# Performance work log

Hardware: AMD Instinct MI355X
Metric: run time of the kernel (lower is better)

## Reference

```python
import jax, jax.numpy as jnp
import numpy as np
from jax import lax

B, S, D, G, V = 32, 8, 128, 32, 64   # batch, slots, hidden_dim, grid_size, vocab_size
K, ED = 128, 32                       # VQ codebook size, code dim


def _conv(x, w, b, pad):
    # standard Conv2d, NCHW / OIHW
    y = lax.conv_general_dilated(x, w, (1, 1), [(pad, pad), (pad, pad)],
                                 dimension_numbers=('NCHW', 'OIHW', 'NCHW'))
    return y + b[None, :, None, None]


def _convT(x, w, b):
    # ConvTranspose2d(k=5, stride=1, padding=2) == conv with spatially flipped
    # kernel, padding k-1-p = 2, channels swapped (IOHW layout of torch weight).
    y = lax.conv_general_dilated(x, jnp.flip(w, (2, 3)), (1, 1), [(2, 2), (2, 2)],
                                 dimension_numbers=('NCHW', 'IOHW', 'NCHW'))
    return y + b[None, :, None, None]


def _build_grid(h, w):
    ys = jnp.linspace(0.0, 1.0, h)
    xs = jnp.linspace(0.0, 1.0, w)
    gy, gx = jnp.meshgrid(ys, xs, indexing='ij')
    g = jnp.stack([gy, gx], axis=-1)                 # [H,W,2]
    return jnp.concatenate([g, 1.0 - g], axis=-1)    # [H,W,4]


def setup_inputs() -> dict:
    key = jax.random.key(0)
    ks = jax.random.split(key, 20)
    sc = 0.05
    n = lambda k, sh: jax.random.normal(k, sh, jnp.float32) * sc
    return {
        'latent': jax.random.normal(ks[0], (B, S, D), jnp.float32),
        'pos_w': n(ks[1], (D, 4)),            # Linear(4, hidden): [out,in]
        'pos_b': jnp.zeros((D,), jnp.float32),
        'ct1_w': n(ks[2], (D, 64, 5, 5)),     # ConvTranspose2d: [in,out,kH,kW]
        'ct1_b': jnp.zeros((64,), jnp.float32),
        'ct2_w': n(ks[3], (64, 32, 5, 5)),
        'ct2_b': jnp.zeros((32,), jnp.float32),
        'codebook': jax.random.uniform(ks[4], (K, ED), jnp.float32, -1.0 / K, 1.0 / K),
        'c1_w': n(ks[5], (64, 32, 3, 3)),     # Conv2d: [out,in,kH,kW]
        'c1_b': jnp.zeros((64,), jnp.float32),
        'c2_w': n(ks[6], (V, 64, 3, 3)),
        'c2_b': jnp.zeros((V,), jnp.float32),
        'a1_w': n(ks[7], (64, 32, 3, 3)),
        'a1_b': jnp.zeros((64,), jnp.float32),
        'a2_w': n(ks[8], (1, 64, 3, 3)),
        'a2_b': jnp.zeros((1,), jnp.float32),
    }


def _forward(latent, pos_w, pos_b, ct1_w, ct1_b, ct2_w, ct2_b, codebook,
             c1_w, c1_b, c2_w, c2_b, a1_w, a1_b, a2_w, a2_b):
    b, s, d = latent.shape
    # spatial broadcast of slot latents -> [B*S, D, H, W]
    z = jnp.broadcast_to(latent.reshape(b * s, d, 1, 1), (b * s, d, G, G))
    # soft position embedding
    grid = _build_grid(G, G)                                  # [H,W,4]
    pos = (grid @ pos_w.T + pos_b).transpose(2, 0, 1)[None]   # [1,D,H,W]
    z = z + pos
    # ConvTranspose decoder
    h = jax.nn.relu(_convT(z, ct1_w, ct1_b))
    feat = jax.nn.relu(_convT(h, ct2_w, ct2_b))               # [B*S,32,H,W]
    # VQ bottleneck on channel-last features
    fp = feat.transpose(0, 2, 3, 1)                           # [B*S,H,W,32]
    flat = fp.reshape(-1, ED)                                 # [N,32]
    dist = (jnp.sum(flat * flat, axis=1, keepdims=True)
            + jnp.sum(codebook * codebook, axis=1)
            - 2.0 * flat @ codebook.T)                        # [N,K]
    idx = jnp.argmin(dist, axis=1)                            # [N]
    q = codebook[idx].reshape(fp.shape)                       # gather lookup
    e_loss = jnp.mean((lax.stop_gradient(q) - fp) ** 2)
    q_loss = jnp.mean((q - lax.stop_gradient(fp)) ** 2)
    vq_loss = q_loss + 0.25 * e_loss
    q_ste = fp + lax.stop_gradient(q - fp)                    # straight-through
    vq_feat = q_ste.transpose(0, 3, 1, 2)                     # [B*S,32,H,W]
    # heads
    colors = _conv(jax.nn.silu(_conv(vq_feat, c1_w, c1_b, 1)), c2_w, c2_b, 1)
    colors = colors.reshape(b, s, V, G, G)
    alphas = _conv(jax.nn.silu(_conv(feat, a1_w, a1_b, 1)), a2_w, a2_b, 1)
    alphas = alphas.reshape(b, s, 1, G, G)
    alphas_n = jax.nn.softmax(alphas, axis=1)
    recon = jnp.sum(alphas_n * colors, axis=1)                # [B,V,H,W]
    return recon, alphas_n, vq_loss


def reference(latent, pos_w, pos_b, ct1_w, ct1_b, ct2_w, ct2_b, codebook,
              c1_w, c1_b, c2_w, c2_b, a1_w, a1_b, a2_w, a2_b):
    return _forward(latent, pos_w, pos_b, ct1_w, ct1_b, ct2_w, ct2_b, codebook,
                    c1_w, c1_b, c2_w, c2_b, a1_w, a1_b, a2_w, a2_b)
```

## Files before the change

### kernel.cpp

```cpp
#include <hip/hip_runtime.h>
#include <math.h>

#define AOFF 2097152
#define LOFF 2359296

typedef __attribute__((ext_vector_type(8))) short short8;
typedef __attribute__((ext_vector_type(4))) float f32x4;

__device__ __forceinline__ int clsf(int v) { return v < 2 ? v : (v > 29 ? v - 27 : 2); }

__device__ __forceinline__ unsigned int f2bfu(float x) {
    unsigned int u = __float_as_uint(x);
    return (u + 0x7FFFu + ((u >> 16) & 1u)) >> 16;
}
__device__ __forceinline__ unsigned int cvt2(float a, float b) {
    return f2bfu(a) | (f2bfu(b) << 16);
}
__device__ __forceinline__ float bf2f(unsigned short u) {
    return __uint_as_float(((unsigned int)u) << 16);
}

__global__ void w1t_kernel(const float* __restrict__ w1, float* __restrict__ w1t) {
    int idx = blockIdx.x * 256 + threadIdx.x;
    if (idx >= 204800) return;
    int tap = idx % 25, rest = idx / 25;
    w1t[tap * 8192 + rest] = w1[idx];
}

__global__ void tapabc_kernel(const float* __restrict__ pw, const float* __restrict__ pb,
                              const float* __restrict__ w1t, float* __restrict__ tapabc) {
    __shared__ float A3[384];
    int tap = blockIdx.x, t = threadIdx.x;
    if (t < 128) {
        float p0 = pw[t * 4], p1 = pw[t * 4 + 1], p2 = pw[t * 4 + 2], p3 = pw[t * 4 + 3];
        A3[t] = p2 + p3 + pb[t];
        A3[128 + t] = p0 - p2;
        A3[256 + t] = p1 - p3;
    }
    __syncthreads();
    int o = t & 63, comp = t >> 6;
    const float* wp = w1t + tap * 8192 + o;
    const float* a = A3 + comp * 128;
    float s = 0.f;
    for (int i = 0; i < 128; ++i) s = fmaf(wp[i * 64], a[i], s);
    tapabc[(tap * 64 + o) * 3 + comp] = s;
}

__global__ void pfill_kernel(const float* __restrict__ tapabc, const float* __restrict__ b1,
                             float* __restrict__ P2) {
    __shared__ float uv[75];
    int o = blockIdx.x, t = threadIdx.x;
    if (t < 75) {
        int cls = t / 3, comp = t % 3;
        int cy = cls / 5, cx = cls % 5;
        const int klo[5] = {2, 1, 0, 0, 0}, khi[5] = {4, 4, 4, 3, 2};
        const float inv31 = 1.f / 31.f;
        float s = (comp == 0) ? b1[o] : 0.f;
        for (int ky = klo[cy]; ky <= khi[cy]; ++ky)
            for (int kx = klo[cx]; kx <= khi[cx]; ++kx) {
                int tap = (4 - ky) * 5 + (4 - kx);
                const float* tp = &tapabc[(tap * 64 + o) * 3];
                if (comp == 0) s += tp[0] + tp[1] * (ky - 2) * inv31 + tp[2] * (kx - 2) * inv31;
                else if (comp == 1) s += tp[1] * inv31;
                else s += tp[2] * inv31;
            }
        uv[t] = s;
    }
    __syncthreads();
    int y = t >> 5, x = t & 31;
    int cls = clsf(y) * 5 + clsf(x);
    float val = uv[cls * 3] + uv[cls * 3 + 1] * y + uv[cls * 3 + 2] * x;
    P2[((o >> 1) << 11) + (t << 1) + (o & 1)] = val;
}

__global__ void wsum_kernel(const float* __restrict__ w1, float* __restrict__ Wsum) {
    int idx = blockIdx.x * 256 + threadIdx.x;
    if (idx >= 25 * 128 * 64) return;
    int cls = idx >> 13;
    int i = (idx >> 6) & 127;
    int o = idx & 63;
    int cy = cls / 5, cx = cls % 5;
    const int klo[5] = {2, 1, 0, 0, 0}, khi[5] = {4, 4, 4, 3, 2};
    float s = 0.f;
    for (int ky = klo[cy]; ky <= khi[cy]; ++ky)
        for (int kx = klo[cx]; kx <= khi[cx]; ++kx)
            s += w1[(i * 64 + o) * 25 + (4 - ky) * 5 + (4 - kx)];
    Wsum[idx] = s;
}

__global__ void m_kernel(const float* __restrict__ latent, const float* __restrict__ Wsum,
                         float* __restrict__ M) {
    int n = blockIdx.x, cls = blockIdx.y, o = threadIdx.x;
    const float* l = &latent[n * 128];
    const float* w = &Wsum[cls * 8192 + o];
    float a0 = 0.f, a1 = 0.f;
    for (int i = 0; i < 128; i += 2) {
        a0 = fmaf(l[i], w[i * 64], a0);
        a1 = fmaf(l[i + 1], w[(i + 1) * 64], a1);
    }
    M[(n * 25 + cls) * 64 + o] = a0 + a1;
}

__global__ void prep_all_kernel(const float* __restrict__ a1w, const float* __restrict__ c1w,
                                const float* __restrict__ c2w, const float* __restrict__ ct2w,
                                short* __restrict__ wtall) {
    int gid = blockIdx.x * 256 + threadIdx.x;
    if (gid < 36864) {
        const float* src = gid < 18432 ? a1w : c1w;
        int idx = gid < 18432 ? gid : gid - 18432;
        int j = idx & 7, fi = idx >> 3;
        int o = fi % 64, g = (fi / 64) & 3, t = fi / 256;
        int i = g * 8 + j;
        wtall[gid] = (short)f2bfu(src[(o * 32 + i) * 9 + (t / 3) * 3 + (t % 3)]);
    } else if (gid < 73728) {
        int idx = gid - 36864;
        int j = idx & 7, fi = idx >> 3;
        int o = fi % 64, g = (fi / 64) & 3, ks = (fi / 256) & 1, t = fi / 512;
        int i = ks * 32 + g * 8 + j;
        wtall[gid] = (short)f2bfu(c2w[(o * 64 + i) * 9 + (t / 3) * 3 + (t % 3)]);
    } else if (gid < 124928) {
        int idx = gid - 73728;
        int j = idx & 7, fi = idx >> 3;
        int o = fi & 31, g = (fi >> 5) & 3, ks = (fi >> 7) & 1, t = fi >> 8;
        int i = ks * 32 + g * 8 + j;
        int ky = t / 5, kx = t % 5;
        wtall[gid] = (short)f2bfu(ct2w[((i * 32 + o) * 5 + (4 - ky)) * 5 + (4 - kx)]);
    }
}

__global__ __launch_bounds__(256) void conv5_kernel(
        const float* __restrict__ M, const float* __restrict__ P2,
        const short* __restrict__ wt, const float* __restrict__ b2,
        unsigned short* __restrict__ featb) {
    __shared__ __align__(16) short tile[12 * 36 * 40];
    __shared__ float Ml[1600];
    const int n = blockIdx.x, y0 = blockIdx.y * 8;
    const int tid = threadIdx.x, w = tid >> 6, l = tid & 63;
    const int lx = l & 15, lg = l >> 4;

    for (int e = tid; e < 1600; e += 256) Ml[e] = M[n * 1600 + e];
    __syncthreads();

    f32x4 acc[2][2][2];
    #pragma unroll
    for (int m = 0; m < 2; ++m)
        #pragma unroll
        for (int q = 0; q < 2; ++q)
            #pragma unroll
            for (int c = 0; c < 2; ++c) acc[m][q][c] = (f32x4){0.f, 0.f, 0.f, 0.f};

    #pragma unroll 1
    for (int ks = 0; ks < 2; ++ks) {
        if (ks) __syncthreads();
        for (int e = tid; e < 6912; e += 256) {
            int cx = e % 36;
            int q = e / 36;
            int ipl = q & 15;
            int r = q >> 4;
            int gy = y0 - 2 + r, gx = cx - 2;
            unsigned int pack = 0u;
            if (gy >= 0 && gy < 32 && gx >= 0 && gx < 32) {
                int cls = clsf(gy) * 5 + clsf(gx);
                int pp = gy * 32 + gx;
                float2 pv = ((const float2*)P2)[((ks * 16 + ipl) << 10) + pp];
                float2 ml = ((const float2*)Ml)[cls * 32 + ks * 16 + ipl];
                pack = cvt2(fmaxf(ml.x + pv.x, 0.f), fmaxf(ml.y + pv.y, 0.f));
            }
            *(unsigned int*)((char*)tile + (r * 36 + cx) * 80 + ipl * 4) = pack;
        }
        __syncthreads();
        for (int kx = 0; kx < 5; ++kx) {
            short8 af[5][2];
            #pragma unroll
            for (int ky = 0; ky < 5; ++ky)
                #pragma unroll
                for (int m = 0; m < 2; ++m)
                    af[ky][m] = *(const short8*)(wt + (ky * 5 + kx) * 2048 +
                                                 ((ks * 4 + lg) * 32 + m * 16 + lx) * 8);
            #pragma unroll
            for (int colf = 0; colf < 2; ++colf) {
                const int cbase = ((2 * w) * 36 + kx + colf * 16 + lx) * 80 + lg * 16;
                short8 bc[6];
                #pragma unroll
                for (int ir = 0; ir < 6; ++ir)
                    bc[ir] = *(const short8*)((char*)tile + cbase + ir * (36 * 80));
                #pragma unroll
                for (int ky = 0; ky < 5; ++ky)
                    #pragma unroll
                    for (int q = 0; q < 2; ++q)
                        #pragma unroll
                        for (int m = 0; m < 2; ++m)
                            acc[m][q][colf] = __builtin_amdgcn_mfma_f32_16x16x32_bf16(
                                af[ky][m], bc[q + ky], acc[m][q][colf], 0, 0, 0);
            }
        }
    }

    #pragma unroll
    for (int m = 0; m < 2; ++m)
        #pragma unroll
        for (int q = 0; q < 2; ++q)
            #pragma unroll
            for (int colf = 0; colf < 2; ++colf) {
                int yl = 2 * w + q, x = colf * 16 + lx;
                unsigned long long pk = 0ull;
                #pragma unroll
                for (int r = 0; r < 4; ++r) {
                    int och = m * 16 + lg * 4 + r;
                    float v = fmaxf(acc[m][q][colf][r] + b2[och], 0.f);
                    pk |= (unsigned long long)f2bfu(v) << (16 * r);
                }
                *(unsigned long long*)(featb + (n * 1024 + (y0 + yl) * 32 + x) * 32
                                       + m * 16 + lg * 4) = pk;
            }
}

template<int ACT>
__global__ __launch_bounds__(256, 6) void conv3_kernel(
        const unsigned short* __restrict__ in_, const short* __restrict__ wt,
        const float* __restrict__ bias, unsigned short* __restrict__ out_) {
    __shared__ __align__(16) short smem[6 * 34 * 40];
    const int n = blockIdx.x, y0 = blockIdx.y * 4;
    const int tid = threadIdx.x, w = tid >> 6, l = tid & 63;
    const int lx = l & 15, lg = l >> 4;

    for (int e = tid; e < 816; e += 256) {
        int px = e >> 2, qc = e & 3;
        int r = px / 34, cx = px - r * 34;
        int gy = y0 - 1 + r, gx = cx - 1;
        short8 v8 = (short8){0, 0, 0, 0, 0, 0, 0, 0};
        if (gy >= 0 && gy < 32 && gx >= 0 && gx < 32)
            v8 = *(const short8*)(in_ + (n * 1024 + gy * 32 + gx) * 32 + qc * 8);
        *(short8*)((char*)smem + px * 80 + qc * 16) = v8;
    }
    __syncthreads();

    f32x4 acc[4][2];
    #pragma unroll
    for (int m = 0; m < 4; ++m)
        #pragma unroll
        for (int c = 0; c < 2; ++c) acc[m][c] = (f32x4){0.f, 0.f, 0.f, 0.f};

    #pragma unroll
    for (int kx = 0; kx < 3; ++kx) {
        short8 bc[2][3];
        #pragma unroll
        for (int colf = 0; colf < 2; ++colf) {
            const int cbase = (w * 34 + kx + colf * 16 + lx) * 80 + lg * 16;
            #pragma unroll
            for (int ir = 0; ir < 3; ++ir)
                bc[colf][ir] = *(const short8*)((char*)smem + cbase + ir * (34 * 80));
        }
        #pragma unroll
        for (int m = 0; m < 4; ++m) {
            short8 af[3];
            #pragma unroll
            for (int ky = 0; ky < 3; ++ky)
                af[ky] = *(const short8*)(wt + (ky * 3 + kx) * 2048 +
                                          (lg * 64 + m * 16 + lx) * 8);
            #pragma unroll
            for (int ky = 0; ky < 3; ++ky)
                #pragma unroll
                for (int colf = 0; colf < 2; ++colf)
                    acc[m][colf] = __builtin_amdgcn_mfma_f32_16x16x32_bf16(
                        af[ky], bc[colf][ky], acc[m][colf], 0, 0, 0);
        }
    }

    #pragma unroll
    for (int m = 0; m < 4; ++m)
        #pragma unroll
        for (int colf = 0; colf < 2; ++colf) {
            int x = colf * 16 + lx;
            unsigned long long pk = 0ull;
            #pragma unroll
            for (int r = 0; r < 4; ++r) {
                int och = m * 16 + lg * 4 + r;
                float v = acc[m][colf][r] + bias[och];
                if (ACT == 1) v = v / (1.f + expf(-v));
                pk |= (unsigned long long)f2bfu(v) << (16 * r);
            }
            *(unsigned long long*)(out_ + (n * 1024 + (y0 + w) * 32 + x) * 64
                                   + m * 16 + lg * 4) = pk;
        }
}

__global__ __launch_bounds__(256) void c2_kernel(
        const unsigned short* __restrict__ in_, const short* __restrict__ wt,
        const float* __restrict__ bias, unsigned short* __restrict__ out_) {
    __shared__ __align__(16) short smem[10 * 34 * 40];
    const int n = blockIdx.x, y0 = blockIdx.y * 8;
    const int tid = threadIdx.x, w = tid >> 6, l = tid & 63;
    const int lx = l & 15, lg = l >> 4;

    short8 r0[6], r1[6];
    int pxv[6], qcv[6];
    #pragma unroll
    for (int it = 0; it < 6; ++it) {
        int e = tid + it * 256;
        int px = e >> 2, qc = e & 3;
        pxv[it] = px; qcv[it] = qc;
        short8 v0 = (short8){0, 0, 0, 0, 0, 0, 0, 0};
        short8 v1 = v0;
        if (e < 1360) {
            int r = px / 34, cx = px - r * 34;
            int gy = y0 - 1 + r, gx = cx - 1;
            if (gy >= 0 && gy < 32 && gx >= 0 && gx < 32) {
                const unsigned short* p = in_ + (n * 1024 + gy * 32 + gx) * 64 + qc * 8;
                v0 = *(const short8*)p;
                v1 = *(const short8*)(p + 32);
            }
        }
        r0[it] = v0; r1[it] = v1;
    }
    #pragma unroll
    for (int it = 0; it < 6; ++it)
        if (tid + it * 256 < 1360)
            *(short8*)((char*)smem + pxv[it] * 80 + qcv[it] * 16) = r0[it];
    __syncthreads();

    f32x4 acc[4][2][2];
    #pragma unroll
    for (int m = 0; m < 4; ++m)
        #pragma unroll
        for (int q = 0; q < 2; ++q)
            #pragma unroll
            for (int c = 0; c < 2; ++c) acc[m][q][c] = (f32x4){0.f, 0.f, 0.f, 0.f};

    #pragma unroll
    for (int kx = 0; kx < 3; ++kx) {
        short8 af[3][4];
        #pragma unroll
        for (int ky = 0; ky < 3; ++ky)
            #pragma unroll
            for (int m = 0; m < 4; ++m)
                af[ky][m] = *(const short8*)(wt + (ky * 3 + kx) * 4096 +
                                             (lg * 64 + m * 16 + lx) * 8);
        #pragma unroll
        for (int colf = 0; colf < 2; ++colf) {
            const int cbase = ((2 * w) * 34 + kx + colf * 16 + lx) * 80 + lg * 16;
            short8 bc[4];
            #pragma unroll
            for (int ir = 0; ir < 4; ++ir)
                bc[ir] = *(const short8*)((char*)smem + cbase + ir * (34 * 80));
            #pragma unroll
            for (int ky = 0; ky < 3; ++ky)
                #pragma unroll
                for (int q = 0; q < 2; ++q)
                    #pragma unroll
                    for (int m = 0; m < 4; ++m)
                        acc[m][q][colf] = __builtin_amdgcn_mfma_f32_16x16x32_bf16(
                            af[ky][m], bc[q + ky], acc[m][q][colf], 0, 0, 0);
        }
    }
    __syncthreads();
    #pragma unroll
    for (int it = 0; it < 6; ++it)
        if (tid + it * 256 < 1360)
            *(short8*)((char*)smem + pxv[it] * 80 + qcv[it] * 16) = r1[it];
    __syncthreads();
    #pragma unroll
    for (int kx = 0; kx < 3; ++kx) {
        short8 af[3][4];
        #pragma unroll
        for (int ky = 0; ky < 3; ++ky)
            #pragma unroll
            for (int m = 0; m < 4; ++m)
                af[ky][m] = *(const short8*)(wt + (ky * 3 + kx) * 4096 +
                                             ((4 + lg) * 64 + m * 16 + lx) * 8);
        #pragma unroll
        for (int colf = 0; colf < 2; ++colf) {
            const int cbase = ((2 * w) * 34 + kx + colf * 16 + lx) * 80 + lg * 16;
            short8 bc[4];
            #pragma unroll
            for (int ir = 0; ir < 4; ++ir)
                bc[ir] = *(const short8*)((char*)smem + cbase + ir * (34 * 80));
            #pragma unroll
            for (int ky = 0; ky < 3; ++ky)
                #pragma unroll
                for (int q = 0; q < 2; ++q)
                    #pragma unroll
                    for (int m = 0; m < 4; ++m)
                        acc[m][q][colf] = __builtin_amdgcn_mfma_f32_16x16x32_bf16(
                            af[ky][m], bc[q + ky], acc[m][q][colf], 0, 0, 0);
        }
    }

    #pragma unroll
    for (int m = 0; m < 4; ++m)
        #pragma unroll
        for (int q = 0; q < 2; ++q)
            #pragma unroll
            for (int colf = 0; colf < 2; ++colf) {
                int yl = 2 * w + q, x = colf * 16 + lx;
                unsigned long long pk = 0ull;
                #pragma unroll
                for (int r = 0; r < 4; ++r) {
                    int och = m * 16 + lg * 4 + r;
                    float v = acc[m][q][colf][r] + bias[och];
                    pk |= (unsigned long long)f2bfu(v) << (16 * r);
                }
                *(unsigned long long*)(out_ + (n * 1024 + (y0 + yl) * 32 + x) * 64
                                       + m * 16 + lg * 4) = pk;
            }
}

__global__ void a2dot_kernel(const unsigned short* __restrict__ in, const float* __restrict__ w,
                             float* __restrict__ s9) {
    __shared__ float wl[576];
    int t = threadIdx.x;
    for (int e = t; e < 576; e += 256) wl[e] = w[e];
    __syncthreads();
    int p = blockIdx.x * 256 + t;
    float acc[9];
    #pragma unroll
    for (int k = 0; k < 9; ++k) acc[k] = 0.f;
    const unsigned short* ip = in + (long long)p * 64;
    #pragma unroll
    for (int c8 = 0; c8 < 8; ++c8) {
        short8 v8 = *(const short8*)(ip + c8 * 8);
        #pragma unroll
        for (int j = 0; j < 8; ++j) {
            float v = bf2f((unsigned short)v8[j]);
            #pragma unroll
            for (int k = 0; k < 9; ++k) acc[k] = fmaf(v, wl[(c8 * 8 + j) * 9 + k], acc[k]);
        }
    }
    #pragma unroll
    for (int k = 0; k < 9; ++k) s9[(k << 18) + p] = acc[k];
}

__global__ void a2soft_kernel(const float* __restrict__ s9, const float* __restrict__ b2,
                              float* __restrict__ outp) {
    int idx = blockIdx.x * 256 + threadIdx.x;
    if (idx >= 32 * 1024) return;
    int bb = idx >> 10, yx = idx & 1023;
    int y = yx >> 5, x = yx & 31;
    float v[8];
    float bias = b2[0];
    #pragma unroll
    for (int s = 0; s < 8; ++s) {
        int n = bb * 8 + s;
        float a = bias;
        #pragma unroll
        for (int ky = 0; ky < 3; ++ky) {
            int yy = y + ky - 1;
            if (yy < 0 || yy > 31) continue;
            #pragma unroll
            for (int kx = 0; kx < 3; ++kx) {
                int xx = x + kx - 1;
                if (xx < 0 || xx > 31) continue;
                a += s9[((ky * 3 + kx) << 18) + (n << 10) + yy * 32 + xx];
            }
        }
        v[s] = a;
    }
    float m = -3.4e38f;
    #pragma unroll
    for (int s = 0; s < 8; ++s) m = fmaxf(m, v[s]);
    float sum = 0.f;
    #pragma unroll
    for (int s = 0; s < 8; ++s) { v[s] = expf(v[s] - m); sum += v[s]; }
    float inv = 1.f / sum;
    #pragma unroll
    for (int s = 0; s < 8; ++s) outp[AOFF + ((bb * 8 + s) << 10) + yx] = v[s] * inv;
}

__global__ __launch_bounds__(256) void vq_mfma_kernel(
        const unsigned short* __restrict__ featb, const float* __restrict__ codebook,
        unsigned short* __restrict__ qfeat, float* __restrict__ partial) {
    __shared__ float cbf[4096];
    __shared__ __align__(16) short cbh[4096];
    __shared__ float cn[128];
    __shared__ float red[4];
    const int tid = threadIdx.x;
    const int w = tid >> 6, l = tid & 63;
    const int lx = l & 15, lg = l >> 4;

    for (int e = tid; e < 4096; e += 256) {
        float v = codebook[e];
        cbf[e] = v;
        int code = e >> 5, d = e & 31;
        int off = (code * 32 + d) * 2;
        off ^= (code & 7) << 4;
        *(short*)((char*)cbh + off) = (short)f2bfu(v);
    }
    __syncthreads();
    if (tid < 128) {
        float s = 0.f;
        #pragma unroll
        for (int c = 0; c < 32; ++c) { float v = cbf[tid * 32 + c]; s = fmaf(v, v, s); }
        cn[tid] = s;
    }
    short8 af[8];
    #pragma unroll
    for (int m = 0; m < 8; ++m) {
        int code = m * 16 + lx;
        int off = (code * 32 + lg * 8) * 2;
        off ^= (code & 7) << 4;
        af[m] = *(const short8*)((char*)cbh + off);
    }
    __syncthreads();
    float cnh[8][4];
    #pragma unroll
    for (int m = 0; m < 8; ++m)
        #pragma unroll
        for (int r = 0; r < 4; ++r)
            cnh[m][r] = 0.5f * cn[m * 16 + lg * 4 + r];

    const int n = blockIdx.x >> 2;
    const int yxw = (blockIdx.x & 3) * 256 + w * 64;
    float lloss = 0.f;

    #pragma unroll 1
    for (int pxg = 0; pxg < 4; ++pxg) {
        int yx = yxw + pxg * 16 + lx;
        short8 bbs = *(const short8*)(featb + (n * 1024 + yx) * 32 + lg * 8);
        f32x4 S[8];
        #pragma unroll
        for (int m = 0; m < 8; ++m)
            S[m] = __builtin_amdgcn_mfma_f32_16x16x32_bf16(
                af[m], bbs, (f32x4){0.f, 0.f, 0.f, 0.f}, 0, 0, 0);
        float bestv = -3.4e38f; int besti = 0;
        #pragma unroll
        for (int m = 0; m < 8; ++m)
            #pragma unroll
            for (int r = 0; r < 4; ++r) {
                float v = S[m][r] - cnh[m][r];
                int code = m * 16 + lg * 4 + r;
                if (v > bestv) { bestv = v; besti = code; }
            }
        #pragma unroll
        for (int d = 16; d < 64; d <<= 1) {
            float ov = __shfl_xor(bestv, d);
            int oi = __shfl_xor(besti, d);
            if (ov > bestv || (ov == bestv && oi < besti)) { bestv = ov; besti = oi; }
        }
        int offq = (besti * 32 + lg * 8) * 2;
        offq ^= (besti & 7) << 4;
        short8 qh = *(const short8*)((char*)cbh + offq);
        *(short8*)(qfeat + (n * 1024 + yx) * 32 + lg * 8) = qh;
        const float* qf = &cbf[besti * 32 + lg * 8];
        #pragma unroll
        for (int j = 0; j < 8; ++j) {
            float fv = bf2f((unsigned short)bbs[j]);
            float dd = qf[j] - fv;
            lloss = fmaf(dd, dd, lloss);
        }
    }
    for (int off = 32; off > 0; off >>= 1) lloss += __shfl_down(lloss, off);
    if (l == 0) red[w] = lloss;
    __syncthreads();
    if (tid == 0) partial[blockIdx.x] = (red[0] + red[1]) + (red[2] + red[3]);
}

__global__ __launch_bounds__(256) void recon_kernel(
        const unsigned short* __restrict__ colors, float* __restrict__ outp) {
    const int b = blockIdx.x, y8 = blockIdx.y;
    const int tid = threadIdx.x;
    const int yxl = tid & 127, vh = tid >> 7;
    const int yx = y8 * 128 + yxl;
    float acc[32];
    #pragma unroll
    for (int v = 0; v < 32; ++v) acc[v] = 0.f;
    #pragma unroll 1
    for (int s = 0; s < 8; ++s) {
        float a = outp[AOFF + ((b * 8 + s) << 10) + yx];
        const unsigned short* cp = colors + ((b * 8 + s) * 1024 + yx) * 64 + vh * 32;
        #pragma unroll
        for (int k = 0; k < 4; ++k) {
            short8 v8 = *(const short8*)(cp + k * 8);
            #pragma unroll
            for (int j = 0; j < 8; ++j)
                acc[k * 8 + j] = fmaf(a, bf2f((unsigned short)v8[j]), acc[k * 8 + j]);
        }
    }
    #pragma unroll
    for (int v = 0; v < 32; ++v)
        outp[(b * 64 + vh * 32 + v) * 1024 + yx] = acc[v];
}

__global__ void loss_kernel(const float* __restrict__ partial, float* __restrict__ outp) {
    __shared__ float red[4];
    int t = threadIdx.x;
    float s = 0.f;
    for (int i = t; i < 1024; i += 256) s += partial[i];
    for (int o = 32; o > 0; o >>= 1) s += __shfl_down(s, o);
    if ((t & 63) == 0) red[t >> 6] = s;
    __syncthreads();
    if (t == 0) outp[LOFF] = 1.25f * ((red[0] + red[1]) + (red[2] + red[3])) / 8388608.0f;
}

extern "C" void kernel_launch(void* const* d_in, const int* in_sizes, int n_in,
                              void* d_out, int out_size, void* d_ws, size_t ws_size,
                              hipStream_t stream) {
    const float* latent  = (const float*)d_in[0];
    const float* pos_w   = (const float*)d_in[1];
    const float* pos_b   = (const float*)d_in[2];
    const float* ct1_w   = (const float*)d_in[3];
    const float* ct1_b   = (const float*)d_in[4];
    const float* ct2_w   = (const float*)d_in[5];
    const float* ct2_b   = (const float*)d_in[6];
    const float* codebook= (const float*)d_in[7];
    const float* c1_w    = (const float*)d_in[8];
    const float* c1_b    = (const float*)d_in[9];
    const float* c2_w    = (const float*)d_in[10];
    const float* c2_b    = (const float*)d_in[11];
    const float* a1_w    = (const float*)d_in[12];
    const float* a1_b    = (const float*)d_in[13];
    const float* a2_w    = (const float*)d_in[14];
    const float* a2_b    = (const float*)d_in[15];
    float* out = (float*)d_out;

    float* ws     = (float*)d_ws;
    unsigned short* featb = (unsigned short*)ws;
    float* s9     = ws + 8388608;
    float* tapabc = s9 + 2359296;
    float* P      = tapabc + 4800;
    float* M      = P + 65536;
    float* partial= M + 409600;
    float* w1t    = partial + 1024;
    float* Wsum   = w1t + 204800;
    short* wtall  = (short*)(Wsum + 204800);
    short* wtA    = wtall;
    short* wtC1   = wtall + 18432;
    short* wtC2   = wtall + 36864;
    short* wtT2   = wtall + 73728;
    unsigned short* tmpb    = (unsigned short*)(wtall + 124928);
    unsigned short* qfeatb  = tmpb + 16777216;
    unsigned short* colorsb = qfeatb + 8388608;

    w1t_kernel<<<800, 256, 0, stream>>>(ct1_w, w1t);
    tapabc_kernel<<<25, 192, 0, stream>>>(pos_w, pos_b, w1t, tapabc);
    pfill_kernel<<<64, 1024, 0, stream>>>(tapabc, ct1_b, P);
    wsum_kernel<<<800, 256, 0, stream>>>(ct1_w, Wsum);
    m_kernel<<<dim3(256, 25), 64, 0, stream>>>(latent, Wsum, M);
    prep_all_kernel<<<488, 256, 0, stream>>>(a1_w, c1_w, c2_w, ct2_w, wtall);

    conv5_kernel<<<dim3(256, 4), 256, 0, stream>>>(M, P, wtT2, ct2_b, featb);
    conv3_kernel<1><<<dim3(256, 8), 256, 0, stream>>>(featb, wtA, a1_b, tmpb);
    a2dot_kernel<<<1024, 256, 0, stream>>>(tmpb, a2_w, s9);
    a2soft_kernel<<<128, 256, 0, stream>>>(s9, a2_b, out);
    vq_mfma_kernel<<<1024, 256, 0, stream>>>(featb, codebook, qfeatb, partial);
    conv3_kernel<1><<<dim3(256, 8), 256, 0, stream>>>(qfeatb, wtC1, c1_b, tmpb);
    c2_kernel<<<dim3(256, 4), 256, 0, stream>>>(tmpb, wtC2, c2_b, colorsb);
    recon_kernel<<<dim3(32, 8), 256, 0, stream>>>(colorsb, out);
    loss_kernel<<<1, 256, 0, stream>>>(partial, out);
}
```

Measured before the change: 226.2 us.

## Fuse alpha conv1 with a2 channel dot and merge weight-prep kernels

A new conv3a2 kernel computes the alpha-head first 3x3 conv with MFMA, applies SiLU, and immediately reduces the 64 channels against the 9 a2 taps using cross-lane shuffles. It writes only the 9 partial sums per pixel, so the 64-channel bf16 intermediate is no longer written to and re-read from global memory and the separate a2dot launch goes away. The w1t transpose kernel is removed by having tapabc gather the weights into shared memory itself, and the Wsum and bf16 weight prep kernels are combined into one launch, cutting launch count. The fused kernel handles 4 rows per block with more register-heavy epilogue work, which could lower occupancy.

```diff
diff --git a/kernel.cpp b/kernel.cpp
--- a/kernel.cpp
+++ b/kernel.cpp
@@ -20,16 +20,10 @@
     return __uint_as_float(((unsigned int)u) << 16);
 }
 
-__global__ void w1t_kernel(const float* __restrict__ w1, float* __restrict__ w1t) {
-    int idx = blockIdx.x * 256 + threadIdx.x;
-    if (idx >= 204800) return;
-    int tap = idx % 25, rest = idx / 25;
-    w1t[tap * 8192 + rest] = w1[idx];
-}
-
 __global__ void tapabc_kernel(const float* __restrict__ pw, const float* __restrict__ pb,
-                              const float* __restrict__ w1t, float* __restrict__ tapabc) {
+                              const float* __restrict__ w1, float* __restrict__ tapabc) {
     __shared__ float A3[384];
+    __shared__ float wl[8192];
     int tap = blockIdx.x, t = threadIdx.x;
     if (t < 128) {
         float p0 = pw[t * 4], p1 = pw[t * 4 + 1], p2 = pw[t * 4 + 2], p3 = pw[t * 4 + 3];
@@ -37,12 +31,12 @@
         A3[128 + t] = p0 - p2;
         A3[256 + t] = p1 - p3;
     }
+    for (int e = t; e < 8192; e += 192) wl[e] = w1[e * 25 + tap];
     __syncthreads();
     int o = t & 63, comp = t >> 6;
-    const float* wp = w1t + tap * 8192 + o;
     const float* a = A3 + comp * 128;
     float s = 0.f;
-    for (int i = 0; i < 128; ++i) s = fmaf(wp[i * 64], a[i], s);
+    for (int i = 0; i < 128; ++i) s = fmaf(wl[i * 64 + o], a[i], s);
     tapabc[(tap * 64 + o) * 3 + comp] = s;
 }
 
@@ -73,38 +67,26 @@
     P2[((o >> 1) << 11) + (t << 1) + (o & 1)] = val;
 }
 
-__global__ void wsum_kernel(const float* __restrict__ w1, float* __restrict__ Wsum) {
-    int idx = blockIdx.x * 256 + threadIdx.x;
-    if (idx >= 25 * 128 * 64) return;
-    int cls = idx >> 13;
-    int i = (idx >> 6) & 127;
-    int o = idx & 63;
-    int cy = cls / 5, cx = cls % 5;
+__global__ void prep_ws_kernel(const float* __restrict__ w1,
+                               const float* __restrict__ a1w, const float* __restrict__ c1w,
+                               const float* __restrict__ c2w, const float* __restrict__ ct2w,
+                               float* __restrict__ Wsum, short* __restrict__ wtall) {
+    int gid = blockIdx.x * 256 + threadIdx.x;
     const int klo[5] = {2, 1, 0, 0, 0}, khi[5] = {4, 4, 4, 3, 2};
-    float s = 0.f;
-    for (int ky = klo[cy]; ky <= khi[cy]; ++ky)
-        for (int kx = klo[cx]; kx <= khi[cx]; ++kx)
-            s += w1[(i * 64 + o) * 25 + (4 - ky) * 5 + (4 - kx)];
-    Wsum[idx] = s;
-}
-
-__global__ void m_kernel(const float* __restrict__ latent, const float* __restrict__ Wsum,
-                         float* __restrict__ M) {
-    int n = blockIdx.x, cls = blockIdx.y, o = threadIdx.x;
-    const float* l = &latent[n * 128];
-    const float* w = &Wsum[cls * 8192 + o];
-    float a0 = 0.f, a1 = 0.f;
-    for (int i = 0; i < 128; i += 2) {
-        a0 = fmaf(l[i], w[i * 64], a0);
-        a1 = fmaf(l[i + 1], w[(i + 1) * 64], a1);
-    }
-    M[(n * 25 + cls) * 64 + o] = a0 + a1;
-}
-
-__global__ void prep_all_kernel(const float* __restrict__ a1w, const float* __restrict__ c1w,
-                                const float* __restrict__ c2w, const float* __restrict__ ct2w,
-                                short* __restrict__ wtall) {
-    int gid = blockIdx.x * 256 + threadIdx.x;
+    if (gid < 204800) {
+        int idx = gid;
+        int cls = idx >> 13;
+        int i = (idx >> 6) & 127;
+        int o = idx & 63;
+        int cy = cls / 5, cx = cls % 5;
+        float s = 0.f;
+        for (int ky = klo[cy]; ky <= khi[cy]; ++ky)
+            for (int kx = klo[cx]; kx <= khi[cx]; ++kx)
+                s += w1[(i * 64 + o) * 25 + (4 - ky) * 5 + (4 - kx)];
+        Wsum[idx] = s;
+        return;
+    }
+    gid -= 204800;
     if (gid < 36864) {
         const float* src = gid < 18432 ? a1w : c1w;
         int idx = gid < 18432 ? gid : gid - 18432;
@@ -128,6 +110,19 @@
     }
 }
 
+__global__ void m_kernel(const float* __restrict__ latent, const float* __restrict__ Wsum,
+                         float* __restrict__ M) {
+    int n = blockIdx.x, cls = blockIdx.y, o = threadIdx.x;
+    const float* l = &latent[n * 128];
+    const float* w = &Wsum[cls * 8192 + o];
+    float a0 = 0.f, a1 = 0.f;
+    for (int i = 0; i < 128; i += 2) {
+        a0 = fmaf(l[i], w[i * 64], a0);
+        a1 = fmaf(l[i + 1], w[(i + 1) * 64], a1);
+    }
+    M[(n * 25 + cls) * 64 + o] = a0 + a1;
+}
+
 __global__ __launch_bounds__(256) void conv5_kernel(
         const float* __restrict__ M, const float* __restrict__ P2,
         const short* __restrict__ wt, const float* __restrict__ b2,
@@ -285,6 +280,97 @@
         }
 }
 
+__global__ __launch_bounds__(256, 4) void conv3a2_kernel(
+        const unsigned short* __restrict__ in_, const short* __restrict__ wt,
+        const float* __restrict__ bias, const float* __restrict__ a2w,
+        float* __restrict__ s9) {
+    __shared__ __align__(16) short smem[6 * 34 * 40];
+    __shared__ float wl9[576];
+    const int n = blockIdx.x, y0 = blockIdx.y * 4;
+    const int tid = threadIdx.x, w = tid >> 6, l = tid & 63;
+    const int lx = l & 15, lg = l >> 4;
+
+    for (int e = tid; e < 576; e += 256) wl9[e] = a2w[e];
+    for (int e = tid; e < 816; e += 256) {
+        int px = e >> 2, qc = e & 3;
+        int r = px / 34, cx = px - r * 34;
+        int gy = y0 - 1 + r, gx = cx - 1;
+        short8 v8 = (short8){0, 0, 0, 0, 0, 0, 0, 0};
+        if (gy >= 0 && gy < 32 && gx >= 0 && gx < 32)
+            v8 = *(const short8*)(in_ + (n * 1024 + gy * 32 + gx) * 32 + qc * 8);
+        *(short8*)((char*)smem + px * 80 + qc * 16) = v8;
+    }
+    __syncthreads();
+
+    f32x4 acc[4][2];
+    #pragma unroll
+    for (int m = 0; m < 4; ++m)
+        #pragma unroll
+        for (int c = 0; c < 2; ++c) acc[m][c] = (f32x4){0.f, 0.f, 0.f, 0.f};
+
+    #pragma unroll
+    for (int kx = 0; kx < 3; ++kx) {
+        short8 bc[2][3];
+        #pragma unroll
+        for (int colf = 0; colf < 2; ++colf) {
+            const int cbase = (w * 34 + kx + colf * 16 + lx) * 80 + lg * 16;
+            #pragma unroll
+            for (int ir = 0; ir < 3; ++ir)
+                bc[colf][ir] = *(const short8*)((char*)smem + cbase + ir * (34 * 80));
+        }
+        #pragma unroll
+        for (int m = 0; m < 4; ++m) {
+            short8 af[3];
+            #pragma unroll
+            for (int ky = 0; ky < 3; ++ky)
+                af[ky] = *(const short8*)(wt + (ky * 3 + kx) * 2048 +
+                                          (lg * 64 + m * 16 + lx) * 8);
+            #pragma unroll
+            for (int ky = 0; ky < 3; ++ky)
+                #pragma unroll
+                for (int colf = 0; colf < 2; ++colf)
+                    acc[m][colf] = __builtin_amdgcn_mfma_f32_16x16x32_bf16(
+                        af[ky], bc[colf][ky], acc[m][colf], 0, 0, 0);
+        }
+    }
+
+    float p9[2][9];
+    #pragma unroll
+    for (int c = 0; c < 2; ++c)
+        #pragma unroll
+        for (int t9 = 0; t9 < 9; ++t9) p9[c][t9] = 0.f;
+    #pragma unroll
+    for (int m = 0; m < 4; ++m)
+        #pragma unroll
+        for (int r = 0; r < 4; ++r) {
+            int och = m * 16 + lg * 4 + r;
+            float wv[9];
+            #pragma unroll
+            for (int t9 = 0; t9 < 9; ++t9) wv[t9] = wl9[och * 9 + t9];
+            float b = bias[och];
+            #pragma unroll
+            for (int colf = 0; colf < 2; ++colf) {
+                float v = acc[m][colf][r] + b;
+                v = v / (1.f + expf(-v));
+                #pragma unroll
+                for (int t9 = 0; t9 < 9; ++t9) p9[colf][t9] = fmaf(v, wv[t9], p9[colf][t9]);
+            }
+        }
+    #pragma unroll
+    for (int d = 16; d < 64; d <<= 1)
+        #pragma unroll
+        for (int colf = 0; colf < 2; ++colf)
+            #pragma unroll
+            for (int t9 = 0; t9 < 9; ++t9)
+                p9[colf][t9] += __shfl_xor(p9[colf][t9], d);
+    if (lg < 2) {
+        int colf = lg;
+        int p = (n << 10) + (y0 + w) * 32 + colf * 16 + lx;
+        #pragma unroll
+        for (int t9 = 0; t9 < 9; ++t9) s9[(t9 << 18) + p] = p9[colf][t9];
+    }
+}
+
 __global__ __launch_bounds__(256) void c2_kernel(
         const unsigned short* __restrict__ in_, const short* __restrict__ wt,
         const float* __restrict__ bias, unsigned short* __restrict__ out_) {
@@ -403,31 +489,6 @@
                 *(unsigned long long*)(out_ + (n * 1024 + (y0 + yl) * 32 + x) * 64
                                        + m * 16 + lg * 4) = pk;
             }
-}
-
-__global__ void a2dot_kernel(const unsigned short* __restrict__ in, const float* __restrict__ w,
-                             float* __restrict__ s9) {
-    __shared__ float wl[576];
-    int t = threadIdx.x;
-    for (int e = t; e < 576; e += 256) wl[e] = w[e];
-    __syncthreads();
-    int p = blockIdx.x * 256 + t;
-    float acc[9];
-    #pragma unroll
-    for (int k = 0; k < 9; ++k) acc[k] = 0.f;
-    const unsigned short* ip = in + (long long)p * 64;
-    #pragma unroll
-    for (int c8 = 0; c8 < 8; ++c8) {
-        short8 v8 = *(const short8*)(ip + c8 * 8);
-        #pragma unroll
-        for (int j = 0; j < 8; ++j) {
-            float v = bf2f((unsigned short)v8[j]);
-            #pragma unroll
-            for (int k = 0; k < 9; ++k) acc[k] = fmaf(v, wl[(c8 * 8 + j) * 9 + k], acc[k]);
-        }
-    }
-    #pragma unroll
-    for (int k = 0; k < 9; ++k) s9[(k << 18) + p] = acc[k];
 }
 
 __global__ void a2soft_kernel(const float* __restrict__ s9, const float* __restrict__ b2,
@@ -619,8 +680,7 @@
     float* P      = tapabc + 4800;
     float* M      = P + 65536;
     float* partial= M + 409600;
-    float* w1t    = partial + 1024;
-    float* Wsum   = w1t + 204800;
+    float* Wsum   = partial + 1024;
     short* wtall  = (short*)(Wsum + 204800);
     short* wtA    = wtall;
     short* wtC1   = wtall + 18432;
@@ -630,16 +690,13 @@
     unsigned short* qfeatb  = tmpb + 16777216;
     unsigned short* colorsb = qfeatb + 8388608;
 
-    w1t_kernel<<<800, 256, 0, stream>>>(ct1_w, w1t);
-    tapabc_kernel<<<25, 192, 0, stream>>>(pos_w, pos_b, w1t, tapabc);
+    tapabc_kernel<<<25, 192, 0, stream>>>(pos_w, pos_b, ct1_w, tapabc);
     pfill_kernel<<<64, 1024, 0, stream>>>(tapabc, ct1_b, P);
-    wsum_kernel<<<800, 256, 0, stream>>>(ct1_w, Wsum);
+    prep_ws_kernel<<<1288, 256, 0, stream>>>(ct1_w, a1_w, c1_w, c2_w, ct2_w, Wsum, wtall);
     m_kernel<<<dim3(256, 25), 64, 0, stream>>>(latent, Wsum, M);
-    prep_all_kernel<<<488, 256, 0, stream>>>(a1_w, c1_w, c2_w, ct2_w, wtall);
 
     conv5_kernel<<<dim3(256, 4), 256, 0, stream>>>(M, P, wtT2, ct2_b, featb);
-    conv3_kernel<1><<<dim3(256, 8), 256, 0, stream>>>(featb, wtA, a1_b, tmpb);
-    a2dot_kernel<<<1024, 256, 0, stream>>>(tmpb, a2_w, s9);
+    conv3a2_kernel<<<dim3(256, 8), 256, 0, stream>>>(featb, wtA, a1_b, a2_w, s9);
     a2soft_kernel<<<128, 256, 0, stream>>>(s9, a2_b, out);
     vq_mfma_kernel<<<1024, 256, 0, stream>>>(featb, codebook, qfeatb, partial);
     conv3_kernel<1><<<dim3(256, 8), 256, 0, stream>>>(qfeatb, wtC1, c1_b, tmpb);
```

Measured after the change: 211.9 us. 6.3% less time.
